# Performance work log

Measured on AMD Instinct MI355X. Metric: run time of the kernel, lower is better.

## Reference

```python
import jax, jax.numpy as jnp
import numpy as np

EPS = 1e-5
B, S, D = 4, 2048, 128
BALL_SCALE = 0.05  # keeps points inside the unit Poincare ball for c=1


def setup_inputs() -> dict:
    key = jax.random.key(0)
    kq, kk, kv = jax.random.split(key, 3)
    q = jax.random.normal(kq, (B, S, D), dtype=jnp.float32) * BALL_SCALE
    k = jax.random.normal(kk, (B, S, D), dtype=jnp.float32) * BALL_SCALE
    v_tangent = jax.random.normal(kv, (B, S, D), dtype=jnp.float32)
    c = jnp.asarray(1.0, dtype=jnp.float32)
    beta = jnp.asarray(0.0, dtype=jnp.float32)            # nn.Parameter init 0.0
    attention_bias = jnp.asarray(0.0, dtype=jnp.float32)  # nn.Parameter init 0.0
    return {"q": q, "k": k, "v_tangent": v_tangent, "c": c,
            "beta": beta, "attention_bias": attention_bias}


def reference(q, k, v_tangent, c, beta, attention_bias):
    sqrt_c = jnp.sqrt(c)

    # --- pairwise Poincare distance (all fp32, as in the torch autocast block) ---
    x_norm_sq = jnp.sum(q * q, axis=-1, keepdims=True)            # (B,S,1)
    y_norm_sq = jnp.sum(k * k, axis=-1, keepdims=True)            # (B,S,1)
    xy_dot = jnp.einsum('bsd,btd->bst', q, k)                     # (B,S,S)
    y_norm_sq_t = jnp.swapaxes(y_norm_sq, -2, -1)                 # (B,1,S)
    diff_norm_sq = x_norm_sq - 2.0 * xy_dot + y_norm_sq_t         # ||x-y||^2, (B,S,S)
    denom = (1.0 - c * x_norm_sq) * (1.0 - c * y_norm_sq_t)       # (B,S,S)
    arg = 1.0 + 2.0 * c * diff_norm_sq / jnp.maximum(denom, EPS)
    dist = jnp.arccosh(jnp.maximum(arg, 1.0 + EPS)) / sqrt_c      # (B,S,S)

    # --- attention ---
    beta_positive = jax.nn.softplus(beta)
    attention_scores = -beta_positive * dist - attention_bias
    attention_weights = jax.nn.softmax(attention_scores, axis=-1)  # (B,S,S)
    output_tangent = jnp.einsum('bst,btd->bsd', attention_weights, v_tangent)

    # --- exp map at origin ---
    v_norm = jnp.maximum(
        jnp.sqrt(jnp.sum(output_tangent * output_tangent, axis=-1, keepdims=True)), EPS)
    output_hyperbolic = (jnp.tanh(sqrt_c * v_norm) / sqrt_c) * (output_tangent / v_norm)

    return output_hyperbolic, attention_weights
```

## Files before the change

kernel.cpp:

```cpp
#include <hip/hip_runtime.h>
#include <math.h>

#define B_ 4
#define S_ 2048
#define D_ 128
#define EPSF 1e-5f
#define BN 128
#define PSB 272

typedef __attribute__((ext_vector_type(8))) short short8;
typedef __attribute__((ext_vector_type(4))) float f32x4;

static __device__ __forceinline__ unsigned short f2bf(float f) {
    unsigned u = __float_as_uint(f);
    return (unsigned short)((u + 0x7fffu + ((u >> 16) & 1u)) >> 16);
}

static __device__ __forceinline__ void gload_lds16(const void* g, void* l) {
    __builtin_amdgcn_global_load_lds((const __attribute__((address_space(1))) unsigned*)g,
                                     (__attribute__((address_space(3))) unsigned*)l, 16, 0, 0);
}


__global__ __launch_bounds__(256) void convqk_kernel(const float* __restrict__ q,
                                                     const float* __restrict__ k,
                                                     const float* __restrict__ cp,
                                                     float* __restrict__ qn, float* __restrict__ kn,
                                                     float* __restrict__ lws,
                                                     float2* __restrict__ qng, float2* __restrict__ kng,
                                                     unsigned* __restrict__ Qb, unsigned* __restrict__ Kb) {
    int row = blockIdx.x * 4 + (threadIdx.x >> 6);
    int lane = threadIdx.x & 63;
    const int NR = B_ * S_;
    const float cc = cp[0];
    bool isQ = row < NR;
    int r = isQ ? row : row - NR;
    float2 v = ((const float2*)(isQ ? q : k))[(size_t)r * 64 + lane];
    unsigned pk = (unsigned)f2bf(v.x) | ((unsigned)f2bf(v.y) << 16);
    float nrm = v.x * v.x + v.y * v.y;
#pragma unroll
    for (int m = 1; m <= 32; m <<= 1) nrm += __shfl_xor(nrm, m, 64);
    if (isQ) {
        Qb[(size_t)r * 64 + lane] = pk;
        if (lane == 0) {
            qn[r] = nrm;
            qng[r] = make_float2(nrm, 2.f * cc * __builtin_amdgcn_rcpf(1.f - cc * nrm));
        }
        if (lane == 1) lws[r] = 0.f;
    } else {
        int c = lane >> 2;
        int cs = c ^ (r & 7);
        Kb[(size_t)r * 64 + cs * 4 + (lane & 3)] = pk;
        if (lane == 0) {
            kn[r] = nrm;
            kng[r] = make_float2(nrm, __builtin_amdgcn_rcpf(1.f - cc * nrm));
        }
    }
}

__global__ __launch_bounds__(256) void convv_kernel(const float* __restrict__ v, uint4* __restrict__ Vtb) {
    __shared__ unsigned short Vs[128 * 132];
    int b = blockIdx.x >> 4;
    int t = blockIdx.x & 15;
    int tid = threadIdx.x;
    const float* src = v + ((size_t)b * S_ + t * 128) * D_;
    int d4 = tid & 31, key0 = tid >> 5;
#pragma unroll
    for (int it = 0; it < 16; ++it) {
        int key = key0 + it * 8;
        float4 f = *(const float4*)(src + (size_t)key * D_ + d4 * 4);
        unsigned short* dst = &Vs[key * 132 + d4 * 4];
        dst[0] = f2bf(f.x); dst[1] = f2bf(f.y); dst[2] = f2bf(f.z); dst[3] = f2bf(f.w);
    }
    __syncthreads();
    uint4* tile = Vtb + (size_t)blockIdx.x * (128 * 16);
    int d = tid & 127;
    int cl = tid >> 7;
#pragma unroll
    for (int it = 0; it < 8; ++it) {
        int c = cl + it * 2;
        int kb = c * 8;
        unsigned short e0 = Vs[(kb + 0) * 132 + d], e1 = Vs[(kb + 1) * 132 + d];
        unsigned short e2 = Vs[(kb + 2) * 132 + d], e3 = Vs[(kb + 3) * 132 + d];
        unsigned short e4 = Vs[(kb + 4) * 132 + d], e5 = Vs[(kb + 5) * 132 + d];
        unsigned short e6 = Vs[(kb + 6) * 132 + d], e7 = Vs[(kb + 7) * 132 + d];
        uint4 o;
        o.x = (unsigned)e0 | ((unsigned)e1 << 16);
        o.y = (unsigned)e2 | ((unsigned)e3 << 16);
        o.z = (unsigned)e4 | ((unsigned)e5 << 16);
        o.w = (unsigned)e6 | ((unsigned)e7 << 16);
        tile[d * 16 + (c ^ (d & 7))] = o;
    }
}


__global__ __launch_bounds__(1024, 4) void hattn4_kernel(
    const unsigned short* __restrict__ Qb, const char* __restrict__ Kb, const char* __restrict__ Vtb,
    const float2* __restrict__ qng, const float2* __restrict__ kng,
    const float* __restrict__ cp, const float* __restrict__ betap, const float* __restrict__ biasp,
    float* __restrict__ hout, float* __restrict__ wout) {

    __shared__ __align__(1024) char smem[142336];
    char* PsB = smem + 131072;
    float* l_row = (float*)(smem + 142080);
    float* nsq_s = (float*)(smem + 142208);

    const int tid = threadIdx.x;
    const int lane = tid & 63, wave = tid >> 6;
    const int wm = wave & 1, wn = wave >> 1;
    const int lm = lane & 15, quad = lane >> 4;

    int xcd = blockIdx.x & 7;
    int b = xcd >> 1;
    int rb = (blockIdx.x >> 3) * 2 + (xcd & 1);
    int s0 = rb * 32;
    const size_t bS = (size_t)b * S_;

    const float beta = betap[0], bias = biasp[0];
    const float cc = cp[0];
    const float beta_pos = fmaxf(beta, 0.f) + log1pf(__expf(-fabsf(beta)));
    const float sqrt_c = sqrtf(cc);
    const float bneg = -beta_pos / sqrt_c;
    const float bias2 = -bias * 1.442695040888963f;
    const float onepe = 1.f + EPSF;

    const char* KbBase = Kb + bS * 256;
    const char* VtBase = Vtb + (size_t)b * 16 * 32768;

    {
#pragma unroll
        for (int j = 0; j < 2; ++j) {
            int m = tid + j * 1024;
            gload_lds16(KbBase + m * 16, smem + m * 16);
            gload_lds16(VtBase + m * 16, smem + 65536 + m * 16);
        }
        if (tid < 128) {
            float2 y = kng[bS + tid];
            *(float2*)(smem + 139776 + tid * 8) = y;
        } else if (tid < 160) {
            float2 x = qng[bS + s0 + (tid - 128)];
            *(float2*)(smem + 141824 + (tid - 128) * 8) = x;
        } else if (tid < 192) {
            l_row[tid - 160] = 0.f;
        } else if (tid < 224) {
            nsq_s[tid - 192] = 0.f;
        }
    }

    short8 aq[4];
    {
        const unsigned short* qrow = Qb + (bS + s0 + wm * 16 + lm) * D_;
#pragma unroll
        for (int ks = 0; ks < 4; ++ks)
            aq[ks] = *(const short8*)(qrow + ks * 32 + quad * 8);
    }

    f32x4 o = {0.f, 0.f, 0.f, 0.f};
    float lacc[4] = {0.f, 0.f, 0.f, 0.f};
    unsigned pst[32];

    __syncthreads();

    int p = 0;
    const int n0 = wn * 16 + lm;
#pragma unroll
    for (int it = 0; it < 16; ++it) {
        char* KsC = smem + p * 32768;
        char* VtC = smem + 65536 + p * 32768;
        const char* YGC = smem + 139776 + p * 1024;

        float2 ygn;
        if (it < 15) {
            const char* ks = KbBase + (size_t)(it + 1) * 32768;
            const char* vs = VtBase + (size_t)(it + 1) * 32768;
            char* kd = smem + (p ^ 1) * 32768;
            char* vd = smem + 65536 + (p ^ 1) * 32768;
#pragma unroll
            for (int j = 0; j < 2; ++j) {
                int off = (tid + j * 1024) * 16;
                gload_lds16(ks + off, kd + off);
                gload_lds16(vs + off, vd + off);
            }
            if (tid < 128) ygn = kng[bS + (size_t)(it + 1) * 128 + tid];
        }

        f32x4 acc = {0.f, 0.f, 0.f, 0.f};
#pragma unroll
        for (int ks = 0; ks < 4; ++ks) {
            int c = ks * 4 + quad;
            short8 bk = *(const short8*)(KsC + n0 * 256 + ((c ^ (n0 & 7)) * 16));
            acc = __builtin_amdgcn_mfma_f32_16x16x32_bf16(aq[ks], bk, acc, 0, 0, 0);
        }

        {
            float2 yg = *(const float2*)(YGC + n0 * 8);
            unsigned pw0 = 0, pw1 = 0;
#pragma unroll
            for (int r = 0; r < 4; ++r) {
                int row = wm * 16 + quad * 4 + r;
                float2 xr = *(const float2*)(smem + 141824 + row * 8);
                float diff = fmaf(-2.f, acc[r], xr.x + yg.x);
                float arg = fmaf(diff * yg.y, xr.y, 1.f);
                arg = fmaxf(arg, onepe);
                float w = arg + sqrtf(fmaf(arg, arg, -1.f));
                float pv = __builtin_amdgcn_exp2f(fmaf(bneg, __builtin_amdgcn_logf(w), bias2));
                unsigned short pb = f2bf(pv);
                *(unsigned short*)(PsB + row * PSB + n0 * 2) = pb;
                lacc[r] += pv;
                if (r == 0) pw0 = pb;
                else if (r == 1) pw0 |= (unsigned)pb << 16;
                else if (r == 2) pw1 = pb;
                else pw1 |= (unsigned)pb << 16;
            }
            pst[it * 2] = pw0;
            pst[it * 2 + 1] = pw1;
        }
        __syncthreads();

        if (it < 15 && tid < 128) *(float2*)(smem + 139776 + (p ^ 1) * 1024 + tid * 8) = ygn;

#pragma unroll
        for (int ks = 0; ks < 4; ++ks) {
            short8 ap = *(const short8*)(PsB + (wm * 16 + lm) * PSB + (ks * 32 + quad * 8) * 2);
            int c = ks * 4 + quad;
            short8 vv = *(const short8*)(VtC + n0 * 256 + ((c ^ (n0 & 7)) * 16));
            o = __builtin_amdgcn_mfma_f32_16x16x32_bf16(ap, vv, o, 0, 0, 0);
        }
        __syncthreads();
        p ^= 1;
    }

#pragma unroll
    for (int r = 0; r < 4; ++r) {
        float s = lacc[r];
#pragma unroll
        for (int m = 1; m <= 8; m <<= 1) s += __shfl_xor(s, m, 64);
        if (lm == 0) atomicAdd(&l_row[wm * 16 + quad * 4 + r], s);
    }
    __syncthreads();

    float linv[4];
#pragma unroll
    for (int r = 0; r < 4; ++r) linv[r] = 1.f / l_row[wm * 16 + quad * 4 + r];

#pragma unroll
    for (int r = 0; r < 4; ++r) {
        float x = o[r] * linv[r];
        o[r] = x;
        float np = x * x;
#pragma unroll
        for (int m = 1; m <= 8; m <<= 1) np += __shfl_xor(np, m, 64);
        if (lm == 0) atomicAdd(&nsq_s[wm * 16 + quad * 4 + r], np);
    }
    __syncthreads();
#pragma unroll
    for (int r = 0; r < 4; ++r) {
        int row = wm * 16 + quad * 4 + r;
        float vn = fmaxf(sqrtf(nsq_s[row]), EPSF);
        float a = sqrt_c * vn;
        float th = 1.f - 2.f / (__expf(2.f * a) + 1.f);
        float sc = th / a;
        hout[(bS + s0 + row) * D_ + n0] = o[r] * sc;
    }

    {
        const size_t wbase = (bS + s0) * (size_t)S_;
        const int row0 = wm * 16 + quad * 4;
#pragma unroll
        for (int it = 0; it < 16; ++it) {
            unsigned pw0 = pst[it * 2], pw1 = pst[it * 2 + 1];
            float p0 = __uint_as_float(pw0 << 16) * linv[0];
            float p1 = __uint_as_float(pw0 & 0xffff0000u) * linv[1];
            float p2 = __uint_as_float(pw1 << 16) * linv[2];
            float p3 = __uint_as_float(pw1 & 0xffff0000u) * linv[3];
            size_t cg = wbase + (size_t)it * 128 + n0;
            wout[cg + (size_t)(row0 + 0) * S_] = p0;
            wout[cg + (size_t)(row0 + 1) * S_] = p1;
            wout[cg + (size_t)(row0 + 2) * S_] = p2;
            wout[cg + (size_t)(row0 + 3) * S_] = p3;
        }
    }
}


__global__ __launch_bounds__(512, 2) void hattn_kernel(
    const unsigned short* __restrict__ Qb, const char* __restrict__ Kb, const char* __restrict__ Vtb,
    const float* __restrict__ qn, const float* __restrict__ kn,
    const float* __restrict__ cp, const float* __restrict__ betap, const float* __restrict__ biasp,
    float* __restrict__ lws, float* __restrict__ houtg, float* __restrict__ woutg) {

    __shared__ __align__(1024) char smem[75136];
    char* KsB = smem;
    char* VtB = smem + 32768;
    char* PsB = smem + 65536;
    float* kn_s  = (float*)(smem + 74240);
    float* qn_s  = (float*)(smem + 74752);
    float* l_row = (float*)(smem + 74880);
    float* nsq_s = (float*)(smem + 75008);

    const int tid = threadIdx.x;
    const int lane = tid & 63, wave = tid >> 6;
    const int wm = wave & 1, wn = wave >> 1;
    const int lm = lane & 15, quad = lane >> 4;

    int xcd = blockIdx.x & 7;
    int b = xcd >> 1;
    int rb = (blockIdx.x >> 3) * 2 + (xcd & 1);
    int s0 = rb * 32;
    const size_t bS = (size_t)b * S_;

    const float cc = cp[0], beta = betap[0], bias = biasp[0];
    const float beta_pos = fmaxf(beta, 0.f) + log1pf(__expf(-fabsf(beta)));
    const float sqrt_c = sqrtf(cc);
    const float inv_sqrt_c = 1.f / sqrt_c;

    if (tid < 32) {
        qn_s[tid] = qn[bS + s0 + tid];
        l_row[tid] = 0.f;
        nsq_s[tid] = 0.f;
    }

    short8 aq[4];
    {
        const unsigned short* qrow = Qb + (bS + s0 + wm * 16 + lm) * D_;
#pragma unroll
        for (int ks = 0; ks < 4; ++ks)
            aq[ks] = *(const short8*)(qrow + ks * 32 + quad * 8);
    }

    f32x4 o0 = {0.f, 0.f, 0.f, 0.f}, o1 = {0.f, 0.f, 0.f, 0.f};

    const char* KbBase = Kb + bS * 256;
    const char* VtBase = Vtb + (size_t)b * 16 * 32768;

    for (int t = 0; t < S_ / BN; ++t) {
        int t0 = t * BN;
        __syncthreads();
        {
            const uint4* ksrc = (const uint4*)(KbBase + (size_t)t0 * 256);
            const uint4* vsrc = (const uint4*)(VtBase + (size_t)t * 32768);
            uint4* kd = (uint4*)KsB;
            uint4* vd = (uint4*)VtB;
#pragma unroll
            for (int i = 0; i < 4; ++i) {
                kd[tid + i * 512] = ksrc[tid + i * 512];
                vd[tid + i * 512] = vsrc[tid + i * 512];
            }
            if (tid < BN) kn_s[tid] = kn[bS + t0 + tid];
        }
        __syncthreads();

        f32x4 acc0 = {0.f, 0.f, 0.f, 0.f}, acc1 = {0.f, 0.f, 0.f, 0.f};
#pragma unroll
        for (int ks = 0; ks < 4; ++ks) {
            int n0 = wn * 32 + lm;
            int c = ks * 4 + quad;
            short8 b0 = *(const short8*)(KsB + n0 * 256 + ((c ^ (n0 & 7)) * 16));
            int n1 = n0 + 16;
            short8 b1 = *(const short8*)(KsB + n1 * 256 + ((c ^ (n1 & 7)) * 16));
            acc0 = __builtin_amdgcn_mfma_f32_16x16x32_bf16(aq[ks], b0, acc0, 0, 0, 0);
            acc1 = __builtin_amdgcn_mfma_f32_16x16x32_bf16(aq[ks], b1, acc1, 0, 0, 0);
        }

        float lp[4];
#pragma unroll
        for (int r = 0; r < 4; ++r) {
            int row = wm * 16 + quad * 4 + r;
            float xn = qn_s[row];
            float fx = 1.f - cc * xn;
            float p0, p1;
#pragma unroll
            for (int nt = 0; nt < 2; ++nt) {
                int col = wn * 32 + nt * 16 + lm;
                float dot = (nt == 0) ? acc0[r] : acc1[r];
                float yn = kn_s[col];
                float diff = xn - 2.f * dot + yn;
                float den = fmaxf(fx * (1.f - cc * yn), EPSF);
                float arg = fmaf(2.f * cc * diff, __builtin_amdgcn_rcpf(den), 1.f);
                arg = fmaxf(arg, 1.f + EPSF);
                float dist = __logf(arg + sqrtf(arg * arg - 1.f)) * inv_sqrt_c;
                float p = __expf(fmaf(-beta_pos, dist, -bias));
                woutg[(bS + s0 + row) * S_ + t0 + col] = p;
                *(unsigned short*)(PsB + row * PSB + col * 2) = f2bf(p);
                if (nt == 0) p0 = p; else p1 = p;
            }
            lp[r] = p0 + p1;
        }
#pragma unroll
        for (int r = 0; r < 4; ++r) {
            float s = lp[r];
#pragma unroll
            for (int m = 1; m <= 8; m <<= 1) s += __shfl_xor(s, m, 64);
            if (lm == 0) atomicAdd(&l_row[wm * 16 + quad * 4 + r], s);
        }
        __syncthreads();

#pragma unroll
        for (int ks = 0; ks < 4; ++ks) {
            short8 ap = *(const short8*)(PsB + (wm * 16 + lm) * PSB + (ks * 32 + quad * 8) * 2);
            int d0 = wn * 32 + lm;
            int c = ks * 4 + quad;
            short8 v0 = *(const short8*)(VtB + d0 * 256 + ((c ^ (d0 & 7)) * 16));
            int d1 = d0 + 16;
            short8 v1 = *(const short8*)(VtB + d1 * 256 + ((c ^ (d1 & 7)) * 16));
            o0 = __builtin_amdgcn_mfma_f32_16x16x32_bf16(ap, v0, o0, 0, 0, 0);
            o1 = __builtin_amdgcn_mfma_f32_16x16x32_bf16(ap, v1, o1, 0, 0, 0);
        }
    }
    __syncthreads();

    float xs0[4], xs1[4];
#pragma unroll
    for (int r = 0; r < 4; ++r) {
        int row = wm * 16 + quad * 4 + r;
        float linv = __builtin_amdgcn_rcpf(l_row[row]);
        float x0 = o0[r] * linv, x1 = o1[r] * linv;
        xs0[r] = x0; xs1[r] = x1;
        float np = x0 * x0 + x1 * x1;
#pragma unroll
        for (int m = 1; m <= 8; m <<= 1) np += __shfl_xor(np, m, 64);
        if (lm == 0) atomicAdd(&nsq_s[row], np);
    }
    if (tid < 32) lws[bS + s0 + tid] = l_row[tid];
    __syncthreads();
#pragma unroll
    for (int r = 0; r < 4; ++r) {
        int row = wm * 16 + quad * 4 + r;
        float vn = fmaxf(sqrtf(nsq_s[row]), EPSF);
        float a = sqrt_c * vn;
        float th = 1.f - 2.f * __builtin_amdgcn_rcpf(__expf(2.f * a) + 1.f);
        float sc = th / a;
        houtg[(bS + s0 + row) * D_ + wn * 32 + lm] = xs0[r] * sc;
        houtg[(bS + s0 + row) * D_ + wn * 32 + 16 + lm] = xs1[r] * sc;
    }
}

__global__ __launch_bounds__(256) void wnorm_kernel(float* __restrict__ w,
                                                    const float* __restrict__ lws) {
    size_t idx = (size_t)blockIdx.x * 256 + threadIdx.x;
    int row = (int)(idx >> 9);
    float linv = 1.f / lws[row];
    float4* p = (float4*)w + idx;
    float4 v = *p;
    v.x *= linv; v.y *= linv; v.z *= linv; v.w *= linv;
    *p = v;
}


extern "C" void kernel_launch(void* const* d_in, const int* in_sizes, int n_in,
                              void* d_out, int out_size, void* d_ws, size_t ws_size,
                              hipStream_t stream) {
    const float* q    = (const float*)d_in[0];
    const float* k    = (const float*)d_in[1];
    const float* v    = (const float*)d_in[2];
    const float* c    = (const float*)d_in[3];
    const float* beta = (const float*)d_in[4];
    const float* ab   = (const float*)d_in[5];

    float* out  = (float*)d_out;
    float* hout = out;
    float* wout = out + (size_t)B_ * S_ * D_;

    float* qn  = (float*)d_ws;
    float* kn  = qn + B_ * S_;
    float* lws = kn + B_ * S_;
    char*  wsb = (char*)d_ws;
    const size_t QG_OFF = 98304;
    const size_t KG_OFF = QG_OFF + 65536;
    const size_t QB_OFF = KG_OFF + 65536;
    const size_t KB_OFF = QB_OFF + 2097152;
    const size_t VT_OFF = KB_OFF + 2097152;
    const size_t NEED1  = VT_OFF + 2097152;

    float2*  qng = (float2*)(wsb + QG_OFF);
    float2*  kng = (float2*)(wsb + KG_OFF);
    unsigned* Qb = (unsigned*)(wsb + QB_OFF);
    unsigned* Kb = (unsigned*)(wsb + KB_OFF);
    uint4*   Vtb = (uint4*)(wsb + VT_OFF);

    if (ws_size >= NEED1) {
        convqk_kernel<<<4096, 256, 0, stream>>>(q, k, c, qn, kn, lws, qng, kng, Qb, Kb);
        convv_kernel<<<64, 256, 0, stream>>>(v, Vtb);
        hattn4_kernel<<<256, 1024, 0, stream>>>((const unsigned short*)Qb, (const char*)Kb,
                                                (const char*)Vtb, qng, kng, c, beta, ab,
                                                hout, wout);
    } else {
        convqk_kernel<<<4096, 256, 0, stream>>>(q, k, c, qn, kn, lws, qng, kng, Qb, Kb);
        convv_kernel<<<64, 256, 0, stream>>>(v, Vtb);
        hattn_kernel<<<256, 512, 0, stream>>>((const unsigned short*)Qb, (const char*)Kb,
                                              (const char*)Vtb, qn, kn, c, beta, ab,
                                              lws, hout, wout);
        wnorm_kernel<<<(B_ * S_ * S_ / 4) / 256, 256, 0, stream>>>(wout, lws);
    }
}
```

Baseline: 150.3 us.

## Spill bf16 probabilities to global workspace and write normalized weights coalesced

```diff
diff --git a/kernel.cpp b/kernel.cpp
--- a/kernel.cpp
+++ b/kernel.cpp
@@ -94,11 +94,11 @@
 }
 
 
-__global__ __launch_bounds__(1024, 4) void hattn4_kernel(
+__global__ __launch_bounds__(1024, 4) void hattn5_kernel(
     const unsigned short* __restrict__ Qb, const char* __restrict__ Kb, const char* __restrict__ Vtb,
     const float2* __restrict__ qng, const float2* __restrict__ kng,
     const float* __restrict__ cp, const float* __restrict__ betap, const float* __restrict__ biasp,
-    float* __restrict__ hout, float* __restrict__ wout) {
+    uint4* __restrict__ Pws, float* __restrict__ hout, float* __restrict__ wout) {
 
     __shared__ __align__(1024) char smem[142336];
     char* PsB = smem + 131072;
@@ -157,13 +157,11 @@
 
     f32x4 o = {0.f, 0.f, 0.f, 0.f};
     float lacc[4] = {0.f, 0.f, 0.f, 0.f};
-    unsigned pst[32];
 
     __syncthreads();
 
     int p = 0;
     const int n0 = wn * 16 + lm;
-#pragma unroll
     for (int it = 0; it < 16; ++it) {
         char* KsC = smem + p * 32768;
         char* VtC = smem + 65536 + p * 32768;
@@ -194,7 +192,6 @@
 
         {
             float2 yg = *(const float2*)(YGC + n0 * 8);
-            unsigned pw0 = 0, pw1 = 0;
 #pragma unroll
             for (int r = 0; r < 4; ++r) {
                 int row = wm * 16 + quad * 4 + r;
@@ -204,20 +201,19 @@
                 arg = fmaxf(arg, onepe);
                 float w = arg + sqrtf(fmaf(arg, arg, -1.f));
                 float pv = __builtin_amdgcn_exp2f(fmaf(bneg, __builtin_amdgcn_logf(w), bias2));
-                unsigned short pb = f2bf(pv);
-                *(unsigned short*)(PsB + row * PSB + n0 * 2) = pb;
+                *(unsigned short*)(PsB + row * PSB + n0 * 2) = f2bf(pv);
                 lacc[r] += pv;
-                if (r == 0) pw0 = pb;
-                else if (r == 1) pw0 |= (unsigned)pb << 16;
-                else if (r == 2) pw1 = pb;
-                else pw1 |= (unsigned)pb << 16;
             }
-            pst[it * 2] = pw0;
-            pst[it * 2 + 1] = pw1;
         }
         __syncthreads();
 
         if (it < 15 && tid < 128) *(float2*)(smem + 139776 + (p ^ 1) * 1024 + tid * 8) = ygn;
+
+        if (tid < 512) {
+            int row = tid >> 4, ch = tid & 15;
+            uint4 pv = *(const uint4*)(PsB + row * PSB + ch * 16);
+            Pws[(((bS + s0 + row) * S_ + (size_t)it * 128) >> 3) + ch] = pv;
+        }
 
 #pragma unroll
         for (int ks = 0; ks < 4; ++ks) {
@@ -264,20 +260,25 @@
     }
 
     {
-        const size_t wbase = (bS + s0) * (size_t)S_;
-        const int row0 = wm * 16 + quad * 4;
-#pragma unroll
-        for (int it = 0; it < 16; ++it) {
-            unsigned pw0 = pst[it * 2], pw1 = pst[it * 2 + 1];
-            float p0 = __uint_as_float(pw0 << 16) * linv[0];
-            float p1 = __uint_as_float(pw0 & 0xffff0000u) * linv[1];
-            float p2 = __uint_as_float(pw1 << 16) * linv[2];
-            float p3 = __uint_as_float(pw1 & 0xffff0000u) * linv[3];
-            size_t cg = wbase + (size_t)it * 128 + n0;
-            wout[cg + (size_t)(row0 + 0) * S_] = p0;
-            wout[cg + (size_t)(row0 + 1) * S_] = p1;
-            wout[cg + (size_t)(row0 + 2) * S_] = p2;
-            wout[cg + (size_t)(row0 + 3) * S_] = p3;
+        const uint4* psrc = Pws + (((bS + s0) * (size_t)S_) >> 3);
+        float4* wdst = (float4*)(wout + (bS + s0) * (size_t)S_);
+#pragma unroll
+        for (int j = 0; j < 8; ++j) {
+            int idx = tid + j * 1024;
+            int row = idx >> 8;
+            float lr = 1.f / l_row[row];
+            uint4 u = psrc[idx];
+            float4 f0, f1;
+            f0.x = __uint_as_float(u.x << 16) * lr;
+            f0.y = __uint_as_float(u.x & 0xffff0000u) * lr;
+            f0.z = __uint_as_float(u.y << 16) * lr;
+            f0.w = __uint_as_float(u.y & 0xffff0000u) * lr;
+            f1.x = __uint_as_float(u.z << 16) * lr;
+            f1.y = __uint_as_float(u.z & 0xffff0000u) * lr;
+            f1.z = __uint_as_float(u.w << 16) * lr;
+            f1.w = __uint_as_float(u.w & 0xffff0000u) * lr;
+            wdst[idx * 2] = f0;
+            wdst[idx * 2 + 1] = f1;
         }
     }
 }
@@ -471,6 +472,8 @@
     const size_t KB_OFF = QB_OFF + 2097152;
     const size_t VT_OFF = KB_OFF + 2097152;
     const size_t NEED1  = VT_OFF + 2097152;
+    const size_t PW_OFF = NEED1;
+    const size_t NEED2  = PW_OFF + (size_t)B_ * S_ * S_ * 2;
 
     float2*  qng = (float2*)(wsb + QG_OFF);
     float2*  kng = (float2*)(wsb + KG_OFF);
@@ -478,12 +481,13 @@
     unsigned* Kb = (unsigned*)(wsb + KB_OFF);
     uint4*   Vtb = (uint4*)(wsb + VT_OFF);
 
-    if (ws_size >= NEED1) {
+    if (ws_size >= NEED2) {
+        uint4* Pws = (uint4*)(wsb + PW_OFF);
         convqk_kernel<<<4096, 256, 0, stream>>>(q, k, c, qn, kn, lws, qng, kng, Qb, Kb);
         convv_kernel<<<64, 256, 0, stream>>>(v, Vtb);
-        hattn4_kernel<<<256, 1024, 0, stream>>>((const unsigned short*)Qb, (const char*)Kb,
+        hattn5_kernel<<<256, 1024, 0, stream>>>((const unsigned short*)Qb, (const char*)Kb,
                                                 (const char*)Vtb, qng, kng, c, beta, ab,
-                                                hout, wout);
+                                                Pws, hout, wout);
     } else {
         convqk_kernel<<<4096, 256, 0, stream>>>(q, k, c, qn, kn, lws, qng, kng, Qb, Kb);
         convv_kernel<<<64, 256, 0, stream>>>(v, Vtb);
```

Measured after the change: 147.6 us. About the same (-1.8%).
